# Kernel optimization log

Measured on AMD Instinct MI355X. Metric: run time of the kernel, lower is better.

Reference implementation:

```python
import jax, jax.numpy as jnp
from jax import lax
import numpy as np

B, S, T = 1024, 512, 48


def setup_inputs() -> dict:
    key = jax.random.key(0)
    k1, k2, k3, k4, k5, k6 = jax.random.split(key, 6)
    emissions = jax.random.normal(k1, (B, S, T), dtype=jnp.float32)
    tags = jax.random.randint(k2, (B, S), 0, T, dtype=jnp.int32)
    # variable-length mask; length >= 1 so position 0 is always valid
    lengths = jax.random.randint(k3, (B,), 1, S + 1, dtype=jnp.int32)
    mask = (jnp.arange(S)[None, :] < lengths[:, None]).astype(jnp.float32)
    transitions = jax.random.normal(k4, (T, T), dtype=jnp.float32)
    start_transitions = jax.random.normal(k5, (T,), dtype=jnp.float32)
    end_transitions = jax.random.normal(k6, (T,), dtype=jnp.float32)
    return {
        "emissions": emissions,
        "tags": tags,
        "mask": mask,
        "transitions": transitions,
        "start_transitions": start_transitions,
        "end_transitions": end_transitions,
    }


def _gold_score(emissions, tags, mask, transitions, start_transitions, end_transitions):
    # score of the gold tag sequence (vectorized over time)
    score = start_transitions[tags[:, 0]]
    score = score + jnp.take_along_axis(emissions[:, 0], tags[:, 0:1], axis=1)[:, 0]
    # NOTE: original code indexes transitions[cur_tag, prev_tag] here (faithful)
    trans_sc = transitions[tags[:, 1:], tags[:, :-1]]                      # [B, S-1]
    emit_sc = jnp.take_along_axis(emissions[:, 1:], tags[:, 1:, None], axis=2)[..., 0]
    score = score + jnp.sum((trans_sc + emit_sc) * mask[:, 1:], axis=1)
    seq_last = mask.sum(axis=1).astype(jnp.int32) - 1                      # [B]
    last_tags = jnp.take_along_axis(tags, seq_last[:, None], axis=1)[:, 0]
    return score + end_transitions[last_tags]


def _forward_algorithm(emissions, mask, transitions, start_transitions, end_transitions):
    # log-partition via logsumexp recurrence, lax.scan over time
    init = start_transitions[None, :] + emissions[:, 0]                    # [B, T]

    def step(score, xs):
        em_i, m_i = xs                                                     # [B,T], [B]
        # next[b, cur] = logsumexp_prev(score[b,prev] + trans[prev,cur] + em[b,cur])
        ns = jax.nn.logsumexp(score[:, :, None] + transitions[None] + em_i[:, None, :], axis=1)
        score = jnp.where(m_i[:, None] > 0, ns, score)
        return score, None

    xs = (jnp.swapaxes(emissions[:, 1:], 0, 1), jnp.swapaxes(mask[:, 1:], 0, 1))
    score, _ = lax.scan(step, init, xs)
    return jax.nn.logsumexp(score + end_transitions[None, :], axis=1)      # [B]


def reference(emissions, tags, mask, transitions, start_transitions, end_transitions):
    gold = _gold_score(emissions, tags, mask, transitions, start_transitions, end_transitions)
    fwd = _forward_algorithm(emissions, mask, transitions, start_transitions, end_transitions)
    return (fwd - gold).mean()
```

## Files before the change

kernel.cpp:

```cpp
#include <hip/hip_runtime.h>


#define T 48
#define SLEN 512
#define BATCH 1024

typedef _Float16 h2 __attribute__((ext_vector_type(2)));

__device__ __forceinline__ float wave_sum(float v) {
#pragma unroll
    for (int m = 32; m >= 1; m >>= 1) v += __shfl_xor(v, m, 64);
    return v;
}
__device__ __forceinline__ float wave_max(float v) {
#pragma unroll
    for (int m = 32; m >= 1; m >>= 1) v = fmaxf(v, __shfl_xor(v, m, 64));
    return v;
}
__device__ __forceinline__ float rlane(float v, int k) {
    return __int_as_float(__builtin_amdgcn_readlane(__float_as_int(v), k));
}
__device__ __forceinline__ float fdot2(h2 a, h2 b, float c) {
#if __has_builtin(__builtin_amdgcn_fdot2)
    return __builtin_amdgcn_fdot2(a, b, c, false);
#else
    return fmaf((float)a[1], (float)b[1], fmaf((float)a[0], (float)b[0], c));
#endif
}

#define QH(S, k) (__builtin_bit_cast(h2, (S)[k]))

#define DOTS48(S, E, A0, A1, A2, A3)                 \
    _Pragma("unroll")                                \
    for (int t = 0; t < 24; t += 4) {                \
        A0 = fdot2(QH(S, t + 0), E[t + 0], A0);      \
        A1 = fdot2(QH(S, t + 1), E[t + 1], A1);      \
        A2 = fdot2(QH(S, t + 2), E[t + 2], A2);      \
        A3 = fdot2(QH(S, t + 3), E[t + 3], A3);      \
    }

#define BCAST24(DST, VAL)                                                 \
    {                                                                     \
        unsigned hp_ = (unsigned)__builtin_bit_cast(unsigned short,       \
                          (_Float16)(VAL));                               \
        unsigned op_ = (unsigned)__builtin_amdgcn_update_dpp(             \
                          (int)hp_, (int)hp_, 0xB1, 0xF, 0xF, false);     \
        unsigned pk_ = (lane & 1) ? (op_ | (hp_ << 16))                   \
                                  : (hp_ | (op_ << 16));                  \
        _Pragma("unroll")                                                 \
        for (int k = 0; k < 24; ++k)                                      \
            (DST)[k] = (unsigned)__builtin_amdgcn_readlane((int)pk_,      \
                                                            2 * k);       \
    }

__global__ __launch_bounds__(128) void crf_kernel(
    const float* __restrict__ em,
    const int*   __restrict__ tags,
    const float* __restrict__ mask,
    const float* __restrict__ trans,
    const float* __restrict__ start_t,
    const float* __restrict__ end_t,
    float*       __restrict__ out)
{
    constexpr float LOG2E = 1.4426950408889634f;
    constexpr float LN2   = 0.6931471805599453f;
    constexpr float ESC   = -8.0f;

    const int b    = blockIdx.x;
    const int tid  = threadIdx.x;
    const int w    = tid >> 6;
    const int lane = tid & 63;
    const int j    = lane < T ? lane : (T - 1);

    const float* em_b   = em   + (size_t)b * SLEN * T;
    const float* mask_b = mask + (size_t)b * SLEN;
    const int*   tags_b = tags + (size_t)b * SLEN;

    float msum = 0.f;
    for (int s = lane; s < SLEN; s += 64) msum += mask_b[s];
    msum = wave_sum(msum);
    const int len = __builtin_amdgcn_readfirstlane((int)(msum + 0.5f));
    const int nb  = (len - 1) >> 1;
    const int nf  = (len - 1) - nb;
    const int steps = w ? nb : nf;

    h2 E[24];
#pragma unroll
    for (int k = 0; k < T; k += 2) {
        const int i0 = w ? (j * T + k)     : (k * T + j);
        const int i1 = w ? (j * T + k + 1) : ((k + 1) * T + j);
        h2 e;
        e[0] = (_Float16)exp2f(trans[i0] * LOG2E + ESC);
        e[1] = (_Float16)exp2f(trans[i1] * LOG2E + ESC);
        E[k >> 1] = e;
    }

    const float* ep = em_b + j;
    const int maxoff = (SLEN - 1) * T;

    float st, L, pubinit;
    if (w == 0) {
        const float z0 = (start_t[j] + em_b[j]) * LOG2E;
        const float m0 = wave_max(z0);
        st = exp2f(z0 - m0); L = m0;
        pubinit = st;
    } else {
        st = exp2f(end_t[j] * LOG2E); L = 0.f;
        const float vlast = ep[(size_t)(len - 1) * T];
        pubinit = fminf(st * exp2f(vlast * LOG2E), 60000.f);
    }
    unsigned sf[24];
    BCAST24(sf, pubinit)

    float g = 0.f;
    if (w == 0) {
        for (int i = lane; i < len; i += 64) {
            if (i >= 1) {
                const int tc = tags_b[i];
                const int tp = tags_b[i - 1];
                g += trans[tc * T + tp] + em_b[(size_t)i * T + tc];
            }
        }
        g = wave_sum(g);
    }

    const int dlt = w ? -T : T;
    int off = w ? (len - 2) * T : T;
    auto ldem = [&]() -> float {
        int oc = off;
        oc = oc < 0 ? 0 : oc;
        oc = oc > maxoff ? maxoff : oc;
        const float r = ep[oc];
        off += dlt;
        return r;
    };
    float fr[16];
#pragma unroll
    for (int k = 0; k < 16; ++k) fr[k] = ldem();

    auto rescale = [&](float& v) {
        float m = fmaxf(fmaxf(rlane(v, 0), rlane(v, 16)),
                        fmaxf(rlane(v, 32), rlane(v, 47)));
        int e = ((__float_as_int(m) >> 23) & 255) - 127;
        e = e < -64 ? -64 : e;
        v *= __int_as_float((127 - e) << 23);
        L += (float)e;
    };

    auto step = [&](float& fe, bool live, bool resc) {
        const float wv = exp2f(fe * LOG2E);
        fe = ldem();
        float a0 = 0.f, a1 = 0.f, a2 = 0.f, a3 = 0.f;
        DOTS48(sf, E, a0, a1, a2, a3)
        float s = (a0 + a1) + (a2 + a3);
        if (w == 0) s *= wv;
        if (live) {
            if (resc) rescale(s);
            st = s;
            const float pub = fminf(w ? s * wv : s, 60000.f);
            BCAST24(sf, pub)
        }
    };

    for (int base = 0; base < steps; base += 16) {
#pragma unroll
        for (int k = 0; k < 16; ++k)
            step(fr[k], (base + k) < steps, ((k & 3) == 3));
    }

    __shared__ float shu[T];
    __shared__ float shL[2];
    if (w == 0) {
        if (lane == 0) shL[0] = L + 8.0f * (float)nf;
    } else {
        if (lane < T) shu[lane] = st;
        if (lane == 0) shL[1] = L + 8.0f * (float)nb;
    }
    __syncthreads();
    if (w == 0) {
        const float v  = (lane < T) ? st * shu[lane] : 0.f;
        const float S_ = wave_sum(v);
        const float fwd = (shL[0] + shL[1] + log2f(S_)) * LN2;
        if (lane == 0) {
            const int t0 = tags_b[0];
            const int tl = tags_b[len - 1];
            const float gold = g + start_t[t0] + em_b[t0] + end_t[tl];
            atomicAdd(out, (fwd - gold) * (1.0f / (float)BATCH));
        }
    }
}

extern "C" void kernel_launch(void* const* d_in, const int* in_sizes, int n_in,
                              void* d_out, int out_size, void* d_ws, size_t ws_size,
                              hipStream_t stream) {
    const float* em      = (const float*)d_in[0];
    const int*   tags    = (const int*)  d_in[1];
    const float* mask    = (const float*)d_in[2];
    const float* trans   = (const float*)d_in[3];
    const float* start_t = (const float*)d_in[4];
    const float* end_t   = (const float*)d_in[5];
    float* out = (float*)d_out;

    hipMemsetAsync(out, 0, sizeof(float), stream);
    crf_kernel<<<BATCH, 128, 0, stream>>>(em, tags, mask, trans, start_t, end_t, out);
}
```

Measured before the change: 239.0 us.

## Batch 16 sequences per block and compute CRF recurrence with MFMA

Result: slower. 395.5 us (+65.5%).

```diff
diff --git a/kernel.cpp b/kernel.cpp
--- a/kernel.cpp
+++ b/kernel.cpp
@@ -4,54 +4,11 @@
 #define T 48
 #define SLEN 512
 #define BATCH 1024
-
-typedef _Float16 h2 __attribute__((ext_vector_type(2)));
-
-__device__ __forceinline__ float wave_sum(float v) {
-#pragma unroll
-    for (int m = 32; m >= 1; m >>= 1) v += __shfl_xor(v, m, 64);
-    return v;
-}
-__device__ __forceinline__ float wave_max(float v) {
-#pragma unroll
-    for (int m = 32; m >= 1; m >>= 1) v = fmaxf(v, __shfl_xor(v, m, 64));
-    return v;
-}
-__device__ __forceinline__ float rlane(float v, int k) {
-    return __int_as_float(__builtin_amdgcn_readlane(__float_as_int(v), k));
-}
-__device__ __forceinline__ float fdot2(h2 a, h2 b, float c) {
-#if __has_builtin(__builtin_amdgcn_fdot2)
-    return __builtin_amdgcn_fdot2(a, b, c, false);
-#else
-    return fmaf((float)a[1], (float)b[1], fmaf((float)a[0], (float)b[0], c));
-#endif
-}
-
-#define QH(S, k) (__builtin_bit_cast(h2, (S)[k]))
-
-#define DOTS48(S, E, A0, A1, A2, A3)                 \
-    _Pragma("unroll")                                \
-    for (int t = 0; t < 24; t += 4) {                \
-        A0 = fdot2(QH(S, t + 0), E[t + 0], A0);      \
-        A1 = fdot2(QH(S, t + 1), E[t + 1], A1);      \
-        A2 = fdot2(QH(S, t + 2), E[t + 2], A2);      \
-        A3 = fdot2(QH(S, t + 3), E[t + 3], A3);      \
-    }
-
-#define BCAST24(DST, VAL)                                                 \
-    {                                                                     \
-        unsigned hp_ = (unsigned)__builtin_bit_cast(unsigned short,       \
-                          (_Float16)(VAL));                               \
-        unsigned op_ = (unsigned)__builtin_amdgcn_update_dpp(             \
-                          (int)hp_, (int)hp_, 0xB1, 0xF, 0xF, false);     \
-        unsigned pk_ = (lane & 1) ? (op_ | (hp_ << 16))                   \
-                                  : (hp_ | (op_ << 16));                  \
-        _Pragma("unroll")                                                 \
-        for (int k = 0; k < 24; ++k)                                      \
-            (DST)[k] = (unsigned)__builtin_amdgcn_readlane((int)pk_,      \
-                                                            2 * k);       \
-    }
+#define NB 16
+#define NBLK (BATCH / NB)
+
+typedef _Float16 f16x8 __attribute__((ext_vector_type(8)));
+typedef float f32x4 __attribute__((ext_vector_type(4)));
 
 __global__ __launch_bounds__(128) void crf_kernel(
     const float* __restrict__ em,
@@ -66,127 +23,246 @@
     constexpr float LN2   = 0.6931471805599453f;
     constexpr float ESC   = -8.0f;
 
-    const int b    = blockIdx.x;
+    const int blk  = blockIdx.x;
     const int tid  = threadIdx.x;
-    const int w    = tid >> 6;
+    const int bwd  = tid >> 6;
     const int lane = tid & 63;
-    const int j    = lane < T ? lane : (T - 1);
-
-    const float* em_b   = em   + (size_t)b * SLEN * T;
-    const float* mask_b = mask + (size_t)b * SLEN;
-    const int*   tags_b = tags + (size_t)b * SLEN;
-
-    float msum = 0.f;
-    for (int s = lane; s < SLEN; s += 64) msum += mask_b[s];
-    msum = wave_sum(msum);
-    const int len = __builtin_amdgcn_readfirstlane((int)(msum + 0.5f));
-    const int nb  = (len - 1) >> 1;
-    const int nf  = (len - 1) - nb;
-    const int steps = w ? nb : nf;
-
-    h2 E[24];
-#pragma unroll
-    for (int k = 0; k < T; k += 2) {
-        const int i0 = w ? (j * T + k)     : (k * T + j);
-        const int i1 = w ? (j * T + k + 1) : ((k + 1) * T + j);
-        h2 e;
-        e[0] = (_Float16)exp2f(trans[i0] * LOG2E + ESC);
-        e[1] = (_Float16)exp2f(trans[i1] * LOG2E + ESC);
-        E[k >> 1] = e;
-    }
-
-    const float* ep = em_b + j;
-    const int maxoff = (SLEN - 1) * T;
-
-    float st, L, pubinit;
-    if (w == 0) {
-        const float z0 = (start_t[j] + em_b[j]) * LOG2E;
-        const float m0 = wave_max(z0);
-        st = exp2f(z0 - m0); L = m0;
-        pubinit = st;
+    const int cl   = lane & 15;
+    const int g    = lane >> 4;
+
+    __shared__ _Float16 trbuf[2][16 * 72];
+    __shared__ float    cmb[64][17];
+    __shared__ float    meta[64];
+
+    for (int i = tid; i < 2 * 16 * 72; i += 128) trbuf[0][i] = (_Float16)0.f;
+
+    {
+        const float* mk = mask + (size_t)(blk * NB + cl) * SLEN;
+        float ms = 0.f;
+        #pragma unroll
+        for (int k = 0; k < SLEN / 16; ++k) {
+            const float4 v = *(const float4*)(mk + g * 4 + 16 * k);
+            ms += (v.x + v.y) + (v.z + v.w);
+        }
+        ms += __shfl_xor(ms, 16, 64);
+        ms += __shfl_xor(ms, 32, 64);
+        if (tid < 16) meta[tid] = ms;
+    }
+    __syncthreads();
+
+    int len_[4], steps_[4];
+    #pragma unroll
+    for (int r = 0; r < 4; ++r) {
+        const int L = (int)(meta[4 * g + r] + 0.5f);
+        len_[r] = L;
+        const int nbk = (L - 1) >> 1;
+        const int nfk = (L - 1) - nbk;
+        steps_[r] = bwd ? nbk : nfk;
+    }
+
+    f16x8 Bop[3][2];
+    #pragma unroll
+    for (int t = 0; t < 3; ++t) {
+        #pragma unroll
+        for (int c = 0; c < 2; ++c) {
+            f16x8 v;
+            #pragma unroll
+            for (int e = 0; e < 8; ++e) {
+                const int kk = 32 * c + g * 8 + e;
+                float tv;
+                if (kk < T) {
+                    const int idx = bwd ? (cl * T + kk)
+                                        : (kk * T + (cl + 16 * t));
+                    tv = exp2f(trans[idx] * LOG2E + ESC);
+                } else {
+                    tv = 0.f;
+                }
+                v[e] = (_Float16)tv;
+            }
+            Bop[t][c] = v;
+        }
+    }
+    if (bwd) {
+        #pragma unroll
+        for (int t = 0; t < 3; ++t) {
+            #pragma unroll
+            for (int c = 0; c < 2; ++c) {
+                f16x8 v;
+                #pragma unroll
+                for (int e = 0; e < 8; ++e) {
+                    const int jj = 32 * c + g * 8 + e;
+                    const int kout = cl + 16 * t;
+                    v[e] = (jj < T)
+                        ? (_Float16)exp2f(trans[kout * T + jj] * LOG2E + ESC)
+                        : (_Float16)0.f;
+                }
+                Bop[t][c] = v;
+            }
+        }
+    }
+
+    const float* bp[4];
+    int noff[4];
+    const int dstep = bwd ? -T : T;
+    const int omax = (SLEN - 1) * T;
+    float D[4][3], snap[4][3], Lr[4], snapL[4];
+    float wA[4][3], wB[4][3];
+    #pragma unroll
+    for (int r = 0; r < 4; ++r) {
+        bp[r] = em + (size_t)(blk * NB + 4 * g + r) * (SLEN * T);
+        Lr[r] = 0.f;
+        #pragma unroll
+        for (int t = 0; t < 3; ++t) {
+            const int ct = cl + 16 * t;
+            D[r][t] = bwd ? exp2f(end_t[ct] * LOG2E)
+                          : exp2f((start_t[ct] + bp[r][ct]) * LOG2E);
+            snap[r][t] = D[r][t];
+        }
+        snapL[r] = 0.f;
+        int o0 = bwd ? (len_[r] - 1) * T : T;
+        o0 = o0 < 0 ? 0 : (o0 > omax ? omax : o0);
+        int o1 = o0 + dstep; o1 = o1 < 0 ? 0 : (o1 > omax ? omax : o1);
+        int o2 = o1 + dstep; o2 = o2 < 0 ? 0 : (o2 > omax ? omax : o2);
+        #pragma unroll
+        for (int t = 0; t < 3; ++t) {
+            wA[r][t] = bp[r][o0 + cl + 16 * t];
+            wB[r][t] = bp[r][o1 + cl + 16 * t];
+        }
+        noff[r] = o2;
+    }
+
+    int mx = steps_[0];
+    #pragma unroll
+    for (int r = 1; r < 4; ++r) mx = steps_[r] > mx ? steps_[r] : mx;
+    #pragma unroll
+    for (int m = 1; m <= 32; m <<= 1) {
+        const int o = __shfl_xor(mx, m, 64);
+        mx = o > mx ? o : mx;
+    }
+    mx = __builtin_amdgcn_readfirstlane(mx);
+
+    _Float16* myt = &trbuf[bwd][0];
+    const int wr0 = 4 * g;
+    const int rd0 = cl * 72 + g * 8;
+
+    auto body = [&](int s, float (&w)[4][3]) {
+        float wx[4][3];
+        #pragma unroll
+        for (int r = 0; r < 4; ++r)
+            #pragma unroll
+            for (int t = 0; t < 3; ++t)
+                wx[r][t] = exp2f(w[r][t] * LOG2E);
+        float Din[4][3];
+        #pragma unroll
+        for (int r = 0; r < 4; ++r)
+            #pragma unroll
+            for (int t = 0; t < 3; ++t)
+                Din[r][t] = bwd ? D[r][t] * wx[r][t] : D[r][t];
+        if ((s & 3) == 3) {
+            #pragma unroll
+            for (int r = 0; r < 4; ++r) {
+                float m = fmaxf(fmaxf(Din[r][0], Din[r][1]), Din[r][2]);
+                #pragma unroll
+                for (int mm = 1; mm <= 8; mm <<= 1)
+                    m = fmaxf(m, __shfl_xor(m, mm, 64));
+                int e = ((__float_as_int(m) >> 23) & 255) - 127;
+                e = e < -64 ? -64 : e;
+                const float sc = __int_as_float((127 - e) << 23);
+                #pragma unroll
+                for (int t = 0; t < 3; ++t) Din[r][t] *= sc;
+                Lr[r] += (float)e;
+            }
+        }
+        #pragma unroll
+        for (int r = 0; r < 4; ++r) {
+            #pragma unroll
+            for (int t = 0; t < 3; ++t) w[r][t] = bp[r][noff[r] + cl + 16 * t];
+            int nn = noff[r] + dstep;
+            noff[r] = nn < 0 ? 0 : (nn > omax ? omax : nn);
+        }
+        #pragma unroll
+        for (int r = 0; r < 4; ++r)
+            #pragma unroll
+            for (int t = 0; t < 3; ++t)
+                myt[(wr0 + r) * 72 + (cl + 16 * t)] =
+                    (_Float16)fminf(Din[r][t], 60000.f);
+        const f16x8 A0 = *(const f16x8*)&myt[rd0];
+        const f16x8 A1 = *(const f16x8*)&myt[rd0 + 32];
+        f32x4 acc0 = {0.f, 0.f, 0.f, 0.f};
+        f32x4 acc1 = {0.f, 0.f, 0.f, 0.f};
+        f32x4 acc2 = {0.f, 0.f, 0.f, 0.f};
+        acc0 = __builtin_amdgcn_mfma_f32_16x16x32_f16(A0, Bop[0][0], acc0, 0, 0, 0);
+        acc1 = __builtin_amdgcn_mfma_f32_16x16x32_f16(A0, Bop[1][0], acc1, 0, 0, 0);
+        acc2 = __builtin_amdgcn_mfma_f32_16x16x32_f16(A0, Bop[2][0], acc2, 0, 0, 0);
+        acc0 = __builtin_amdgcn_mfma_f32_16x16x32_f16(A1, Bop[0][1], acc0, 0, 0, 0);
+        acc1 = __builtin_amdgcn_mfma_f32_16x16x32_f16(A1, Bop[1][1], acc1, 0, 0, 0);
+        acc2 = __builtin_amdgcn_mfma_f32_16x16x32_f16(A1, Bop[2][1], acc2, 0, 0, 0);
+        #pragma unroll
+        for (int r = 0; r < 4; ++r) {
+            float v0 = acc0[r], v1 = acc1[r], v2 = acc2[r];
+            if (!bwd) { v0 *= wx[r][0]; v1 *= wx[r][1]; v2 *= wx[r][2]; }
+            D[r][0] = v0; D[r][1] = v1; D[r][2] = v2;
+            if (steps_[r] - 1 == s) {
+                snap[r][0] = v0; snap[r][1] = v1; snap[r][2] = v2;
+                snapL[r] = Lr[r];
+            }
+        }
+    };
+
+    for (int s = 0; s < mx; s += 2) {
+        body(s, wA);
+        body(s + 1, wB);
+    }
+
+    if (bwd) {
+        #pragma unroll
+        for (int r = 0; r < 4; ++r) {
+            #pragma unroll
+            for (int t = 0; t < 3; ++t) cmb[lane][r * 3 + t] = snap[r][t];
+            cmb[lane][12 + r] = snapL[r];
+        }
     } else {
-        st = exp2f(end_t[j] * LOG2E); L = 0.f;
-        const float vlast = ep[(size_t)(len - 1) * T];
-        pubinit = fminf(st * exp2f(vlast * LOG2E), 60000.f);
-    }
-    unsigned sf[24];
-    BCAST24(sf, pubinit)
-
-    float g = 0.f;
-    if (w == 0) {
-        for (int i = lane; i < len; i += 64) {
-            if (i >= 1) {
-                const int tc = tags_b[i];
-                const int tp = tags_b[i - 1];
-                g += trans[tc * T + tp] + em_b[(size_t)i * T + tc];
-            }
-        }
-        g = wave_sum(g);
-    }
-
-    const int dlt = w ? -T : T;
-    int off = w ? (len - 2) * T : T;
-    auto ldem = [&]() -> float {
-        int oc = off;
-        oc = oc < 0 ? 0 : oc;
-        oc = oc > maxoff ? maxoff : oc;
-        const float r = ep[oc];
-        off += dlt;
-        return r;
-    };
-    float fr[16];
-#pragma unroll
-    for (int k = 0; k < 16; ++k) fr[k] = ldem();
-
-    auto rescale = [&](float& v) {
-        float m = fmaxf(fmaxf(rlane(v, 0), rlane(v, 16)),
-                        fmaxf(rlane(v, 32), rlane(v, 47)));
-        int e = ((__float_as_int(m) >> 23) & 255) - 127;
-        e = e < -64 ? -64 : e;
-        v *= __int_as_float((127 - e) << 23);
-        L += (float)e;
-    };
-
-    auto step = [&](float& fe, bool live, bool resc) {
-        const float wv = exp2f(fe * LOG2E);
-        fe = ldem();
-        float a0 = 0.f, a1 = 0.f, a2 = 0.f, a3 = 0.f;
-        DOTS48(sf, E, a0, a1, a2, a3)
-        float s = (a0 + a1) + (a2 + a3);
-        if (w == 0) s *= wv;
-        if (live) {
-            if (resc) rescale(s);
-            st = s;
-            const float pub = fminf(w ? s * wv : s, 60000.f);
-            BCAST24(sf, pub)
-        }
-    };
-
-    for (int base = 0; base < steps; base += 16) {
-#pragma unroll
-        for (int k = 0; k < 16; ++k)
-            step(fr[k], (base + k) < steps, ((k & 3) == 3));
-    }
-
-    __shared__ float shu[T];
-    __shared__ float shL[2];
-    if (w == 0) {
-        if (lane == 0) shL[0] = L + 8.0f * (float)nf;
-    } else {
-        if (lane < T) shu[lane] = st;
-        if (lane == 0) shL[1] = L + 8.0f * (float)nb;
+        const int bb = blk * NB + cl;
+        const float* eb = em + (size_t)bb * (SLEN * T);
+        const int* tb = tags + (size_t)bb * SLEN;
+        const int Lb_ = (int)(meta[cl] + 0.5f);
+        float gg = 0.f;
+        for (int i = 1 + g; i < Lb_; i += 4) {
+            const int tc = tb[i], tp = tb[i - 1];
+            gg += trans[tc * T + tp] + eb[(size_t)i * T + tc];
+        }
+        if (g == 0) {
+            const int t0 = tb[0], tl = tb[Lb_ - 1];
+            gg += start_t[t0] + eb[t0] + end_t[tl];
+        }
+        gg += __shfl_xor(gg, 16, 64);
+        gg += __shfl_xor(gg, 32, 64);
+        if (g == 0) meta[16 + cl] = gg;
     }
     __syncthreads();
-    if (w == 0) {
-        const float v  = (lane < T) ? st * shu[lane] : 0.f;
-        const float S_ = wave_sum(v);
-        const float fwd = (shL[0] + shL[1] + log2f(S_)) * LN2;
-        if (lane == 0) {
-            const int t0 = tags_b[0];
-            const int tl = tags_b[len - 1];
-            const float gold = g + start_t[t0] + em_b[t0] + end_t[tl];
-            atomicAdd(out, (fwd - gold) * (1.0f / (float)BATCH));
-        }
+
+    if (!bwd) {
+        float contrib = 0.f;
+        #pragma unroll
+        for (int r = 0; r < 4; ++r) {
+            float v = snap[r][0] * cmb[lane][r * 3 + 0]
+                    + snap[r][1] * cmb[lane][r * 3 + 1]
+                    + snap[r][2] * cmb[lane][r * 3 + 2];
+            #pragma unroll
+            for (int mm = 1; mm <= 8; mm <<= 1) v += __shfl_xor(v, mm, 64);
+            const int L = len_[r];
+            const int nbk = (L - 1) >> 1;
+            const int nfk = (L - 1) - nbk;
+            const float fwd = (snapL[r] + cmb[lane][12 + r]
+                               + 8.0f * (float)(nfk + nbk) + log2f(v)) * LN2;
+            const float gold = meta[16 + 4 * g + r];
+            contrib += (fwd - gold);
+        }
+        contrib *= (1.0f / (float)BATCH);
+        contrib = (cl == 0) ? contrib : 0.f;
+        #pragma unroll
+        for (int m = 1; m <= 32; m <<= 1) contrib += __shfl_xor(contrib, m, 64);
+        if (lane == 0) atomicAdd(out, contrib);
     }
 }
 
@@ -202,5 +278,5 @@
     float* out = (float*)d_out;
 
     hipMemsetAsync(out, 0, sizeof(float), stream);
-    crf_kernel<<<BATCH, 128, 0, stream>>>(em, tags, mask, trans, start_t, end_t, out);
+    crf_kernel<<<NBLK, 128, 0, stream>>>(em, tags, mask, trans, start_t, end_t, out);
 }
```
